# Performance work log

Measured on AMD Instinct MI355X. Metric: run time of the kernel, lower is better.

Reference implementation:

```python
import jax, jax.numpy as jnp
import numpy as np

GRID_SIZE = 8
POS_LAMBDA = 250.0
POS_MARGIN = 1.0
NEG_MARGIN = 0.2
N, C, H, W = 2, 256, 48, 64


def setup_inputs() -> dict:
    key = jax.random.key(0)
    k1, k2, k3 = jax.random.split(key, 3)
    desc1 = jax.random.normal(k1, (N, C, H, W), dtype=jnp.float32)
    desc2 = jax.random.normal(k2, (N, C, H, W), dtype=jnp.float32)
    # near-identity homography so the warp stays well-conditioned
    homo = jnp.eye(3, dtype=jnp.float32) + 0.01 * jax.random.normal(k3, (3, 3), dtype=jnp.float32)
    return {"desc1": desc1, "desc2": desc2, "homo": homo}


def _create_grid(n, h, w, dtype):
    # cell-center pixel coordinates, (x, y) order in the last dim
    gy, gx = jnp.meshgrid(jnp.arange(h, dtype=dtype), jnp.arange(w, dtype=dtype), indexing="ij")
    g = jnp.stack([gx, gy], axis=-1) * GRID_SIZE + GRID_SIZE // 2  # [h, w, 2]
    return jnp.broadcast_to(g, (n, h, w, 2))


def _warp_grid(grid, homo):
    ones = jnp.ones(grid.shape[:-1] + (1,), grid.dtype)
    pts = jnp.concatenate([grid, ones], axis=-1)          # [n, h, w, 3]
    wp = jnp.einsum("nhwc,rc->nhwr", pts, homo)           # apply H to homogeneous pts
    return wp[..., :2] / wp[..., 2:3]


def reference(desc1, desc2, homo):
    n, c, h, w = desc1.shape
    grid = _create_grid(n, h, w, desc1.dtype)             # [n, h, w, 2]
    w_grid = _warp_grid(grid, homo)                       # [n, h, w, 2]
    # all-pairs distance between source cell centers and warped cell centers
    diff = grid[:, :, :, None, None, :] - w_grid[:, None, None, :, :, :]  # [n,h,w,h,w,2]
    grid_dist = jnp.linalg.norm(diff, axis=-1)            # [n, h, w, h, w]
    s = (grid_dist <= GRID_SIZE - 0.5).astype(desc1.dtype)
    # dense all-pairs descriptor correlation (contraction over C)
    dot_desc = jnp.einsum("nchw,ncij->nhwij", desc1, desc2)  # [n, h, w, h, w]
    pos_dist = jnp.maximum(POS_MARGIN - dot_desc, 0.0)
    neg_dist = jnp.maximum(dot_desc - NEG_MARGIN, 0.0)
    loss = POS_LAMBDA * s * pos_dist + (1.0 - s) * neg_dist
    return loss.mean()
```

## Files before the change

kernel.cpp:

```cpp
#include <hip/hip_runtime.h>


#define GS 8
#define POS_LAMBDA 250.0f
#define POS_MARGIN 1.0f
#define NEG_MARGIN 0.2f
#define N_ 2
#define C_ 256
#define H_ 48
#define W_ 64
#define P_ (H_ * W_)
#define R2_THRESH 56.25f

#define BM 128
#define BN 128
#define BK 64
#define TM (P_ / BM)
#define TN (P_ / BN)
#define GEMM_BLOCKS (N_ * TM * TN)

typedef __attribute__((ext_vector_type(8))) short short8;
typedef __attribute__((ext_vector_type(4))) float floatx4;

__device__ __forceinline__ unsigned short f32_to_bf16(float f) {
    unsigned u = __builtin_bit_cast(unsigned, f);
    unsigned r = (u + 0x7FFFu + ((u >> 16) & 1u)) >> 16;
    return (unsigned short)r;
}

__device__ __forceinline__ void load16_to_lds(const void* g, void* l) {
    __builtin_amdgcn_global_load_lds(
        (const __attribute__((address_space(1))) void*)g,
        (__attribute__((address_space(3))) void*)l, 16, 0, 0);
}

__global__ __launch_bounds__(256) void prep_kernel(const float* __restrict__ in1,
                                                   const float* __restrict__ in2,
                                                   const float* __restrict__ homo,
                                                   unsigned short* __restrict__ o1,
                                                   unsigned short* __restrict__ o2,
                                                   float* __restrict__ wg) {
    int bid = blockIdx.x;
    int t = threadIdx.x;

    if (bid < 12) {
        int p = bid * 256 + t;
        float gx = (float)((p & (W_ - 1)) * GS + GS / 2);
        float gy = (float)((p >> 6) * GS + GS / 2);
        float h0 = homo[0], h1 = homo[1], h2 = homo[2];
        float h3 = homo[3], h4 = homo[4], h5 = homo[5];
        float h6 = homo[6], h7 = homo[7], h8 = homo[8];
        float w0 = fmaf(h0, gx, fmaf(h1, gy, h2));
        float w1 = fmaf(h3, gx, fmaf(h4, gy, h5));
        float w2 = fmaf(h6, gx, fmaf(h7, gy, h8));
        wg[2 * p]     = w0 / w2;
        wg[2 * p + 1] = w1 / w2;
        return;
    }

    int b = bid - 12;
    int d = b & 1;
    int r = b >> 1;
    int n = r / (48 * 4);
    int r2 = r % (48 * 4);
    int pt = r2 >> 2;
    int ct = r2 & 3;
    const float* src = (d ? in2 : in1) + ((size_t)n * C_ + ct * 64) * P_ + pt * 64;
    unsigned short* dst = (d ? o2 : o1) + ((size_t)n * P_ + (size_t)pt * 64) * C_ + ct * 64;

    __shared__ unsigned short tile[64][72];

#pragma unroll
    for (int i = 0; i < 4; ++i) {
        int idx = t + i * 256;
        int c = idx >> 4;
        int p4 = (idx & 15) << 2;
        float4 v = *(const float4*)(src + (size_t)c * P_ + p4);
        tile[p4 + 0][c] = f32_to_bf16(v.x);
        tile[p4 + 1][c] = f32_to_bf16(v.y);
        tile[p4 + 2][c] = f32_to_bf16(v.z);
        tile[p4 + 3][c] = f32_to_bf16(v.w);
    }
    __syncthreads();
#pragma unroll
    for (int i = 0; i < 2; ++i) {
        int idx = t + i * 256;
        int p = idx >> 3;
        int c8 = (idx & 7) << 3;
        *(short8*)(dst + (size_t)p * C_ + c8) = *(const short8*)&tile[p][c8];
    }
}

__global__ __launch_bounds__(256) void mfma_hinge_kernel(const unsigned short* __restrict__ bf1,
                                                         const unsigned short* __restrict__ bf2,
                                                         const float* __restrict__ wg,
                                                         const float* __restrict__ homo,
                                                         float* __restrict__ partial) {
    __shared__ __attribute__((aligned(16))) char smem[32768];
    __shared__ float red[4];

    const int bid = (blockIdx.x & 7) * (GEMM_BLOCKS / 8) + (blockIdx.x >> 3);
    const int n   = bid / (TM * TN);
    const int rem = bid % (TM * TN);
    const int bp1 = (rem / TN) * BM;
    const int bp2 = (rem % TN) * BN;
    const unsigned short* A = bf1 + (size_t)n * P_ * C_;
    const unsigned short* B = bf2 + (size_t)n * P_ * C_;

    const int t    = threadIdx.x;
    const int lane = t & 63;
    const int wv   = t >> 6;
    const int wr   = wv >> 1;
    const int wc   = wv & 1;
    const int sub  = lane >> 3;
    const int slot = lane & 7;
    const int c16  = slot ^ sub;

    floatx4 acc[4][4];
#pragma unroll
    for (int i = 0; i < 4; ++i)
#pragma unroll
        for (int j = 0; j < 4; ++j)
            acc[i][j] = floatx4{0.0f, 0.0f, 0.0f, 0.0f};

    for (int k0 = 0; k0 < C_; k0 += BK) {
        if (k0) __syncthreads();
#pragma unroll
        for (int i = 0; i < 4; ++i) {
            int chunk = wv * 4 + i;
            int row = chunk * 8 + sub;
            load16_to_lds((const char*)(A + (size_t)(bp1 + row) * C_ + k0) + c16 * 16,
                          smem + chunk * 1024);
        }
#pragma unroll
        for (int i = 0; i < 4; ++i) {
            int chunk = wv * 4 + i;
            int row = chunk * 8 + sub;
            load16_to_lds((const char*)(B + (size_t)(bp2 + row) * C_ + k0) + c16 * 16,
                          smem + 16384 + chunk * 1024);
        }
        __syncthreads();

#pragma unroll
        for (int kk = 0; kk < 2; ++kk) {
            short8 af[4], bfr[4];
#pragma unroll
            for (int i = 0; i < 4; ++i) {
                int row = wr * 64 + i * 16 + (lane & 15);
                int q   = kk * 4 + (lane >> 4);
                int off = row * 128 + ((q ^ (row & 7)) << 4);
                af[i] = *(const short8*)(smem + off);
            }
#pragma unroll
            for (int j = 0; j < 4; ++j) {
                int row = wc * 64 + j * 16 + (lane & 15);
                int q   = kk * 4 + (lane >> 4);
                int off = row * 128 + ((q ^ (row & 7)) << 4);
                bfr[j] = *(const short8*)(smem + 16384 + off);
            }
#pragma unroll
            for (int i = 0; i < 4; ++i)
#pragma unroll
                for (int j = 0; j < 4; ++j)
                    acc[i][j] = __builtin_amdgcn_mfma_f32_16x16x32_bf16(af[i], bfr[j],
                                                                        acc[i][j], 0, 0, 0);
        }
    }

    bool skip;
    {
        float h3 = homo[3], h4 = homo[4], h5 = homo[5];
        float h6 = homo[6], h7 = homo[7], h8 = homo[8];
        float y2a = (float)((bp2 >> 6) * GS + GS / 2);
        float y2b = y2a + 8.0f;
        float wymin = 1e30f, wymax = -1e30f;
        bool ok = true;
#pragma unroll
        for (int cidx = 0; cidx < 4; ++cidx) {
            float x = (cidx & 1) ? 508.0f : 4.0f;
            float y = (cidx & 2) ? y2b : y2a;
            float w2 = fmaf(h6, x, fmaf(h7, y, h8));
            ok = ok && (w2 > 1e-6f);
            float wy = fmaf(h3, x, fmaf(h4, y, h5)) / w2;
            wymin = fminf(wymin, wy);
            wymax = fmaxf(wymax, wy);
        }
        float y1min = (float)((bp1 >> 6) * GS + GS / 2);
        float y1max = y1min + 8.0f;
        skip = ok && ((y1max < wymin - 7.6f) || (y1min > wymax + 7.6f));
    }

    const int col   = lane & 15;
    const int rbase = (lane >> 4) * 4;
    float lsum = 0.0f;
    if (skip) {
#pragma unroll
        for (int j = 0; j < 4; ++j)
#pragma unroll
            for (int i = 0; i < 4; ++i)
#pragma unroll
                for (int r = 0; r < 4; ++r)
                    lsum += fmaxf(acc[i][j][r] - NEG_MARGIN, 0.0f);
    } else {
#pragma unroll
        for (int j = 0; j < 4; ++j) {
            int p2 = bp2 + wc * 64 + j * 16 + col;
            float wx = wg[2 * p2], wy = wg[2 * p2 + 1];
#pragma unroll
            for (int i = 0; i < 4; ++i) {
                int p1b = bp1 + wr * 64 + i * 16 + rbase;
#pragma unroll
                for (int r = 0; r < 4; ++r) {
                    int p1 = p1b + r;
                    float gx = (float)((p1 & (W_ - 1)) * GS + GS / 2);
                    float gy = (float)((p1 >> 6) * GS + GS / 2);
                    float dx = gx - wx, dy = gy - wy;
                    float r2 = fmaf(dx, dx, dy * dy);
                    float dot = acc[i][j][r];
                    float pos = fmaxf(POS_MARGIN - dot, 0.0f);
                    float neg = fmaxf(dot - NEG_MARGIN, 0.0f);
                    lsum += (r2 <= R2_THRESH) ? POS_LAMBDA * pos : neg;
                }
            }
        }
    }

#pragma unroll
    for (int off = 32; off > 0; off >>= 1)
        lsum += __shfl_down(lsum, off, 64);
    if (lane == 0) red[wv] = lsum;
    __syncthreads();
    if (t == 0) partial[bid] = red[0] + red[1] + red[2] + red[3];
}

__global__ __launch_bounds__(256) void reduce_kernel(const float* __restrict__ partial,
                                                     float* __restrict__ out) {
    __shared__ double sd[256];
    int t = threadIdx.x;
    double s = 0.0;
    for (int i = t; i < GEMM_BLOCKS; i += 256) s += (double)partial[i];
    sd[t] = s;
    __syncthreads();
    for (int off = 128; off > 0; off >>= 1) {
        if (t < off) sd[t] += sd[t + off];
        __syncthreads();
    }
    if (t == 0) {
        double cnt = (double)N_ * (double)P_ * (double)P_;
        out[0] = (float)(sd[0] / cnt);
    }
}

extern "C" void kernel_launch(void* const* d_in, const int* in_sizes, int n_in,
                              void* d_out, int out_size, void* d_ws, size_t ws_size,
                              hipStream_t stream) {
    const float* desc1 = (const float*)d_in[0];
    const float* desc2 = (const float*)d_in[1];
    const float* homo  = (const float*)d_in[2];
    float* out = (float*)d_out;

    unsigned short* b1 = (unsigned short*)d_ws;
    unsigned short* b2 = b1 + (size_t)N_ * P_ * C_;
    float* partial = (float*)(b2 + (size_t)N_ * P_ * C_);
    float* wgbuf   = partial + GEMM_BLOCKS;

    prep_kernel<<<780, 256, 0, stream>>>(desc1, desc2, homo, b1, b2, wgbuf);
    mfma_hinge_kernel<<<GEMM_BLOCKS, 256, 0, stream>>>(b1, b2, wgbuf, homo, partial);
    reduce_kernel<<<1, 256, 0, stream>>>(partial, out);
}
```

Before: 32.82 us.

## Double-buffer LDS tiles with BK=32 to overlap global loads with MFMA

Halves the K tile to 32 and splits the same 32 KB of LDS into two buffers, so the next K slice is prefetched via global_load_lds while the current one feeds the MFMAs. The goal is to hide global-to-LDS latency that the single-buffer loop exposed between two barriers. The swizzle and read offsets are reworked for 64-byte rows. In exchange there are twice as many K iterations and barriers, each with less MFMA work. Because the prefetch is an async direct-to-LDS load, overlap depends on how the compiler places its wait counts before the barrier.

```diff
diff --git a/kernel.cpp b/kernel.cpp
--- a/kernel.cpp
+++ b/kernel.cpp
@@ -14,10 +14,12 @@
 
 #define BM 128
 #define BN 128
-#define BK 64
+#define BK 32
+#define NKSTEPS (C_ / BK)
 #define TM (P_ / BM)
 #define TN (P_ / BN)
 #define GEMM_BLOCKS (N_ * TM * TN)
+#define BUFSZ 16384
 
 typedef __attribute__((ext_vector_type(8))) short short8;
 typedef __attribute__((ext_vector_type(4))) float floatx4;
@@ -96,7 +98,7 @@
                                                          const float* __restrict__ wg,
                                                          const float* __restrict__ homo,
                                                          float* __restrict__ partial) {
-    __shared__ __attribute__((aligned(16))) char smem[32768];
+    __shared__ __attribute__((aligned(16))) char smem[2 * BUFSZ];
     __shared__ float red[4];
 
     const int bid = (blockIdx.x & 7) * (GEMM_BLOCKS / 8) + (blockIdx.x >> 3);
@@ -112,9 +114,11 @@
     const int wv   = t >> 6;
     const int wr   = wv >> 1;
     const int wc   = wv & 1;
-    const int sub  = lane >> 3;
-    const int slot = lane & 7;
-    const int c16  = slot ^ sub;
+
+    const int srow = lane >> 2;
+    const int sc16 = (lane & 3) ^ ((lane >> 3) & 3);
+
+    const int rslot = ((lane >> 4) ^ ((lane >> 1) & 3)) << 4;
 
     floatx4 acc[4][4];
 #pragma unroll
@@ -123,49 +127,53 @@
         for (int j = 0; j < 4; ++j)
             acc[i][j] = floatx4{0.0f, 0.0f, 0.0f, 0.0f};
 
-    for (int k0 = 0; k0 < C_; k0 += BK) {
-        if (k0) __syncthreads();
+#define STAGE_TILES(buf, k0)                                                          \
+    do {                                                                              \
+        _Pragma("unroll")                                                             \
+        for (int i_ = 0; i_ < 2; ++i_) {                                              \
+            int chunk = wv * 2 + i_;                                                  \
+            int row = chunk * 16 + srow;                                              \
+            load16_to_lds((const char*)(A + (size_t)(bp1 + row) * C_ + (k0)) + sc16 * 16, \
+                          smem + (buf) * BUFSZ + chunk * 1024);                       \
+        }                                                                             \
+        _Pragma("unroll")                                                             \
+        for (int i_ = 0; i_ < 2; ++i_) {                                              \
+            int chunk = wv * 2 + i_;                                                  \
+            int row = chunk * 16 + srow;                                              \
+            load16_to_lds((const char*)(B + (size_t)(bp2 + row) * C_ + (k0)) + sc16 * 16, \
+                          smem + (buf) * BUFSZ + 8192 + chunk * 1024);                \
+        }                                                                             \
+    } while (0)
+
+    STAGE_TILES(0, 0);
+    __syncthreads();
+
+    for (int kt = 0; kt < NKSTEPS; ++kt) {
+        const char* cur = smem + (kt & 1) * BUFSZ;
+        if (kt < NKSTEPS - 1)
+            STAGE_TILES((kt + 1) & 1, (kt + 1) * BK);
+
+        short8 af[4], bfr[4];
 #pragma unroll
         for (int i = 0; i < 4; ++i) {
-            int chunk = wv * 4 + i;
-            int row = chunk * 8 + sub;
-            load16_to_lds((const char*)(A + (size_t)(bp1 + row) * C_ + k0) + c16 * 16,
-                          smem + chunk * 1024);
-        }
-#pragma unroll
-        for (int i = 0; i < 4; ++i) {
-            int chunk = wv * 4 + i;
-            int row = chunk * 8 + sub;
-            load16_to_lds((const char*)(B + (size_t)(bp2 + row) * C_ + k0) + c16 * 16,
-                          smem + 16384 + chunk * 1024);
-        }
+            int row = wr * 64 + i * 16 + (lane & 15);
+            af[i] = *(const short8*)(cur + row * 64 + rslot);
+        }
+#pragma unroll
+        for (int j = 0; j < 4; ++j) {
+            int row = wc * 64 + j * 16 + (lane & 15);
+            bfr[j] = *(const short8*)(cur + 8192 + row * 64 + rslot);
+        }
+#pragma unroll
+        for (int i = 0; i < 4; ++i)
+#pragma unroll
+            for (int j = 0; j < 4; ++j)
+                acc[i][j] = __builtin_amdgcn_mfma_f32_16x16x32_bf16(af[i], bfr[j],
+                                                                    acc[i][j], 0, 0, 0);
+
         __syncthreads();
-
-#pragma unroll
-        for (int kk = 0; kk < 2; ++kk) {
-            short8 af[4], bfr[4];
-#pragma unroll
-            for (int i = 0; i < 4; ++i) {
-                int row = wr * 64 + i * 16 + (lane & 15);
-                int q   = kk * 4 + (lane >> 4);
-                int off = row * 128 + ((q ^ (row & 7)) << 4);
-                af[i] = *(const short8*)(smem + off);
-            }
-#pragma unroll
-            for (int j = 0; j < 4; ++j) {
-                int row = wc * 64 + j * 16 + (lane & 15);
-                int q   = kk * 4 + (lane >> 4);
-                int off = row * 128 + ((q ^ (row & 7)) << 4);
-                bfr[j] = *(const short8*)(smem + 16384 + off);
-            }
-#pragma unroll
-            for (int i = 0; i < 4; ++i)
-#pragma unroll
-                for (int j = 0; j < 4; ++j)
-                    acc[i][j] = __builtin_amdgcn_mfma_f32_16x16x32_bf16(af[i], bfr[j],
-                                                                        acc[i][j], 0, 0, 0);
-        }
-    }
+    }
+#undef STAGE_TILES
 
     bool skip;
     {
```

Measured after the change: 34.78 us. 1.06x slower.
